# Optimization experiments

Measured on AMD Instinct MI355X. Metric: run time of the kernel, lower is better.

The kernel has to match this reference:

```python
import jax, jax.numpy as jnp
import numpy as np

K = 1024      # num_embeddings
D = 256       # embedding_dim
BETA = 0.25


def setup_inputs() -> dict:
    key = jax.random.key(0)
    k1, k2 = jax.random.split(key)
    z = jax.random.normal(k1, (4, D, 16, 32, 32), dtype=jnp.float32)
    # matches torch init: uniform(-1/K, 1/K)
    embedding = jax.random.uniform(k2, (K, D), dtype=jnp.float32,
                                   minval=-1.0 / K, maxval=1.0 / K)
    return {"z": z, "embedding": embedding}


def reference(z, embedding):
    # z: (B, C, Dd, H, W) with C == D
    z_perm = jnp.transpose(z, (0, 2, 3, 4, 1))          # (B, Dd, H, W, C)
    flat = z_perm.reshape(-1, D)                        # (N, D)

    dist = (jnp.sum(flat * flat, axis=1, keepdims=True)
            + jnp.sum(embedding * embedding, axis=1)
            - 2.0 * flat @ embedding.T)
    indices_flat = jnp.argmin(dist, axis=1)             # (N,)

    # one-hot @ embedding == direct gather
    z_q_flat = embedding[indices_flat]                  # (N, D)
    z_q = z_q_flat.reshape(z_perm.shape)

    commitment_loss = jnp.mean((z_perm - jax.lax.stop_gradient(z_q)) ** 2)
    vq_loss = BETA * commitment_loss

    # straight-through estimator
    z_q_st = z_perm + jax.lax.stop_gradient(z_q - z_perm)
    z_q_out = jnp.transpose(z_q_st, (0, 4, 1, 2, 3))    # back to (B, C, Dd, H, W)

    # perplexity from assignment histogram
    n = flat.shape[0]
    counts = jnp.zeros((K,), dtype=flat.dtype).at[indices_flat].add(1.0)
    avg_probs = counts / n
    perplexity = jnp.exp(-jnp.sum(avg_probs * jnp.log(avg_probs + 1e-10)))

    indices = indices_flat.reshape(z_perm.shape[:-1])   # (B, Dd, H, W)
    return z_q_out, vq_loss, indices, perplexity
```

## Files before the change

kernel.cpp:

```cpp
#include <hip/hip_runtime.h>

#define Dd 256
#define Kc 1024
#define SPATIAL 16384
#define NROWS 65536
#define NELEM 16777216
#define LOSS_OFF 16777216
#define IDX_OFF  16777217
#define PERP_OFF (16777217 + 65536)
#define MARGIN 3.5e-4f

typedef _Float16 f16x8 __attribute__((ext_vector_type(8)));
typedef _Float16 f16x2 __attribute__((ext_vector_type(2)));
typedef float f32x4 __attribute__((ext_vector_type(4)));


__global__ __launch_bounds__(256) void prep2_kernel(const float* __restrict__ emb,
                                                    _Float16* __restrict__ ef,
                                                    float* __restrict__ se) {
  const int j = blockIdx.x, c = threadIdx.x;
  float v = emb[j * Dd + c];
  ef[j * Dd + c] = (_Float16)(v * 1024.0f);
  double s = (double)v * (double)v;
  #pragma unroll
  for (int off = 32; off; off >>= 1) s += __shfl_down(s, off, 64);
  __shared__ double ws4[4];
  if ((threadIdx.x & 63) == 0) ws4[threadIdx.x >> 6] = s;
  __syncthreads();
  if (threadIdx.x == 0) se[j] = (float)(ws4[0] + ws4[1] + ws4[2] + ws4[3]);
}

__global__ __launch_bounds__(256, 2) void prefilter2_kernel(const float* __restrict__ z,
                                                            const _Float16* __restrict__ ef,
                                                            const float* __restrict__ se,
                                                            float* __restrict__ sx,
                                                            float* __restrict__ rowmin,
                                                            int* __restrict__ candcount,
                                                            int* __restrict__ cand_g) {
  __shared__ _Float16 As[32 * 272];
  __shared__ double sxp[8][32];
  __shared__ float selds[Kc];
  __shared__ int cnts[32];
  __shared__ int cands[32][8];
  __shared__ float rminw[4][32];
  __shared__ float rthr[32];

  const int tid = threadIdx.x;
  const int n0 = blockIdx.x * 32;
  const int b = n0 >> 14, s0 = n0 & 16383;
  const float* zb = z + (size_t)b * (Dd * SPATIAL) + s0;

  {
    const int r = tid & 31, cp = tid >> 5;
    double acc = 0.0;
    #pragma unroll 8
    for (int c = cp * 32; c < cp * 32 + 32; ++c) {
      const float v = zb[(size_t)c * SPATIAL + r];
      As[r * 272 + c] = (_Float16)v;
      acc += (double)v * (double)v;
    }
    sxp[cp][r] = acc;
  }
  #pragma unroll
  for (int i = 0; i < 4; ++i) selds[tid + 256 * i] = se[tid + 256 * i];
  if (tid < 32) cnts[tid] = 0;
  __syncthreads();
  if (tid < 32) {
    double s = 0.0;
    #pragma unroll
    for (int p = 0; p < 8; ++p) s += sxp[p][tid];
    sx[n0 + tid] = (float)s;
  }

  const int w = tid >> 6, lane = tid & 63, q = lane >> 4, l15 = lane & 15;
  const int colbase = w * 256;

  f16x8 Afrag[2][8];
  #pragma unroll
  for (int rt = 0; rt < 2; ++rt)
    #pragma unroll
    for (int kk = 0; kk < 8; ++kk)
      Afrag[rt][kk] = *(const f16x8*)(&As[(rt * 16 + l15) * 272 + kk * 32 + q * 8]);

  const _Float16* efb = ef + (size_t)(colbase + l15) * Dd + q * 8;

  float rmin8[8];
  #pragma unroll
  for (int i = 0; i < 8; ++i) rmin8[i] = 3.4e38f;
  f16x2 scst[16][4];

  #pragma unroll
  for (int ct = 0; ct < 16; ++ct) {
    const _Float16* bp = efb + (size_t)ct * 16 * Dd;
    f16x8 B[8];
    #pragma unroll
    for (int kk = 0; kk < 8; ++kk) B[kk] = *(const f16x8*)(bp + kk * 32);
    f32x4 a0 = {0.f, 0.f, 0.f, 0.f}, a1 = {0.f, 0.f, 0.f, 0.f};
    #pragma unroll
    for (int kk = 0; kk < 8; ++kk) {
      a0 = __builtin_amdgcn_mfma_f32_16x16x32_f16(Afrag[0][kk], B[kk], a0, 0, 0, 0);
      a1 = __builtin_amdgcn_mfma_f32_16x16x32_f16(Afrag[1][kk], B[kk], a1, 0, 0, 0);
    }
    const float sec = selds[colbase + ct * 16 + l15];
    #pragma unroll
    for (int reg = 0; reg < 4; ++reg) {
      const float sc0 = fmaf(-0.001953125f, a0[reg], sec);
      const float sc1 = fmaf(-0.001953125f, a1[reg], sec);
      rmin8[reg]     = fminf(rmin8[reg], sc0);
      rmin8[reg + 4] = fminf(rmin8[reg + 4], sc1);
      scst[ct][reg] = (f16x2){(_Float16)sc0, (_Float16)sc1};
    }
  }

  #pragma unroll
  for (int m = 1; m <= 8; m <<= 1)
    #pragma unroll
    for (int i = 0; i < 8; ++i) rmin8[i] = fminf(rmin8[i], __shfl_xor(rmin8[i], m, 64));
  if (l15 == 0) {
    #pragma unroll
    for (int reg = 0; reg < 4; ++reg) {
      rminw[w][q * 4 + reg] = rmin8[reg];
      rminw[w][16 + q * 4 + reg] = rmin8[4 + reg];
    }
  }
  __syncthreads();
  if (tid < 32) {
    const float m = fminf(fminf(rminw[0][tid], rminw[1][tid]),
                          fminf(rminw[2][tid], rminw[3][tid]));
    rowmin[n0 + tid] = m;
    rthr[tid] = m + MARGIN;
  }
  __syncthreads();

  float thr0[4], thr1[4];
  #pragma unroll
  for (int reg = 0; reg < 4; ++reg) {
    thr0[reg] = rthr[q * 4 + reg];
    thr1[reg] = rthr[16 + q * 4 + reg];
  }
  #pragma unroll
  for (int ct = 0; ct < 16; ++ct) {
    const int col = colbase + ct * 16 + l15;
    #pragma unroll
    for (int reg = 0; reg < 4; ++reg) {
      if ((float)scst[ct][reg][0] < thr0[reg]) {
        const int pos = atomicAdd(&cnts[q * 4 + reg], 1);
        if (pos < 8) cands[q * 4 + reg][pos] = col;
      }
      if ((float)scst[ct][reg][1] < thr1[reg]) {
        const int pos = atomicAdd(&cnts[16 + q * 4 + reg], 1);
        if (pos < 8) cands[16 + q * 4 + reg][pos] = col;
      }
    }
  }
  __syncthreads();
  if (tid < 32) candcount[n0 + tid] = cnts[tid];
  cand_g[(size_t)(n0 + (tid >> 3)) * 8 + (tid & 7)] = cands[tid >> 3][tid & 7];
}

__global__ __launch_bounds__(256) void resolve_easy_kernel(const int* __restrict__ candcount,
                                                           const int* __restrict__ cand_g,
                                                           const float* __restrict__ sx,
                                                           const float* __restrict__ rowmin,
                                                           float* __restrict__ out_idx_f,
                                                           int* __restrict__ idx_i,
                                                           int* __restrict__ counts,
                                                           int* __restrict__ hardcnt,
                                                           int* __restrict__ hardlist,
                                                           double* __restrict__ loss_sum) {
  const int tid = threadIdx.x;
  const int n = blockIdx.x * 256 + tid;
  const int cnt = candcount[n];
  double lp = 0.0;
  if (cnt == 1) {
    const int j = cand_g[(size_t)n * 8];
    idx_i[n] = j;
    out_idx_f[n] = (float)j;
    atomicAdd(&counts[j], 1);
    lp = (double)sx[n] + (double)rowmin[n];
  } else {
    const int pos = atomicAdd(hardcnt, 1);
    hardlist[pos] = n;
  }
  #pragma unroll
  for (int off = 32; off; off >>= 1) lp += __shfl_down(lp, off, 64);
  __shared__ double dred[4];
  if ((tid & 63) == 0) dred[tid >> 6] = lp;
  __syncthreads();
  if (tid == 0) atomicAdd(loss_sum, dred[0] + dred[1] + dred[2] + dred[3]);
}

__global__ __launch_bounds__(256) void resolve_hard_kernel(const float* __restrict__ z,
                                                           const float* __restrict__ emb,
                                                           const float* __restrict__ se,
                                                           const float* __restrict__ sx,
                                                           const int* __restrict__ candcount,
                                                           const int* __restrict__ cand_g,
                                                           const int* __restrict__ hardcnt,
                                                           const int* __restrict__ hardlist,
                                                           float* __restrict__ out_idx_f,
                                                           int* __restrict__ idx_i,
                                                           int* __restrict__ counts,
                                                           double* __restrict__ loss_sum) {
  __shared__ float xs[4][256];
  const int tid = threadIdx.x, w = tid >> 6, lane = tid & 63;
  const int hc = *hardcnt;
  const int nw = gridDim.x * 4;
  double wloss = 0.0;
  for (int i = blockIdx.x * 4 + w; i < hc; i += nw) {
    const int n = hardlist[i];
    const int b = n >> 14, s = n & 16383;
    #pragma unroll
    for (int ro = 0; ro < 4; ++ro)
      xs[w][ro * 64 + lane] =
          z[(size_t)b * (Dd * SPATIAL) + (size_t)(ro * 64 + lane) * SPATIAL + s];
    asm volatile("s_waitcnt lgkmcnt(0) vmcnt(0)" ::: "memory");
    const int cnt = candcount[n];
    const float sxn = sx[n];
    float scb = 3.4e38f;
    int jb = 0x7fffffff;
    if (cnt <= 8) {
      if (lane < cnt) {
        jb = cand_g[(size_t)n * 8 + lane];
        const float4* ep = (const float4*)(emb + (size_t)jb * Dd);
        float acc = 0.f;
        #pragma unroll 8
        for (int kk = 0; kk < 64; ++kk) {
          const float4 e4 = ep[kk];
          const float* xp = &xs[w][kk * 4];
          acc = fmaf(xp[0], e4.x, acc);
          acc = fmaf(xp[1], e4.y, acc);
          acc = fmaf(xp[2], e4.z, acc);
          acc = fmaf(xp[3], e4.w, acc);
        }
        const float t1 = sxn + se[jb];
        scb = t1 - 2.0f * acc;
      }
    } else {
      for (int jj = 0; jj < 16; ++jj) {
        const int j = lane * 16 + jj;
        const float4* ep = (const float4*)(emb + (size_t)j * Dd);
        float acc = 0.f;
        #pragma unroll 8
        for (int kk = 0; kk < 64; ++kk) {
          const float4 e4 = ep[kk];
          const float* xp = &xs[w][kk * 4];
          acc = fmaf(xp[0], e4.x, acc);
          acc = fmaf(xp[1], e4.y, acc);
          acc = fmaf(xp[2], e4.z, acc);
          acc = fmaf(xp[3], e4.w, acc);
        }
        const float t1 = sxn + se[j];
        const float sc = t1 - 2.0f * acc;
        if (sc < scb) { scb = sc; jb = j; }
      }
    }
    #pragma unroll
    for (int m = 1; m <= 32; m <<= 1) {
      const float so = __shfl_xor(scb, m, 64);
      const int jo = __shfl_xor(jb, m, 64);
      if (so < scb || (so == scb && jo < jb)) { scb = so; jb = jo; }
    }
    if (lane == 0) {
      idx_i[n] = jb;
      out_idx_f[n] = (float)jb;
      atomicAdd(&counts[jb], 1);
      wloss += (double)sxn + (double)scb;
    }
  }
  if (lane == 0) atomicAdd(loss_sum, wloss);
}

__global__ __launch_bounds__(256) void phase2c_kernel(const float* __restrict__ emb,
                                                      const int* __restrict__ idx_i,
                                                      float* __restrict__ out_zq) {
  __shared__ float els[64 * 257];
  __shared__ int sidx[64];
  const int tid = threadIdx.x;
  const int blk = blockIdx.x, b = blk >> 8, s0 = (blk & 255) << 6;
  if (tid < 64) sidx[tid] = idx_i[b * SPATIAL + s0 + tid];
  __syncthreads();
  {
    const int rr = tid >> 2, p = tid & 3;
    const float* ep = emb + (size_t)sidx[rr] * Dd + p * 64;
    float* dl = els + rr * 257 + p * 64;
    #pragma unroll
    for (int i = 0; i < 64; i += 4) {
      const float4 e4 = *(const float4*)(ep + i);
      dl[i] = e4.x; dl[i + 1] = e4.y; dl[i + 2] = e4.z; dl[i + 3] = e4.w;
    }
  }
  __syncthreads();
  const int s = tid & 63, coff = tid >> 6;
  const size_t zb = (size_t)b * (Dd * SPATIAL);
  #pragma unroll 4
  for (int c = coff; c < Dd; c += 4)
    out_zq[zb + (size_t)c * SPATIAL + s0 + s] = els[s * 257 + c];
}

__global__ __launch_bounds__(256) void finalize_kernel(const int* __restrict__ counts,
                                                       const double* __restrict__ loss_sum,
                                                       float* __restrict__ out) {
  const int tid = threadIdx.x;
  double local = 0.0;
  for (int k = tid; k < Kc; k += 256) {
    const double p = (double)counts[k] / (double)NROWS;
    local += p * log(p + 1e-10);
  }
  #pragma unroll
  for (int off = 32; off; off >>= 1) local += __shfl_down(local, off, 64);
  __shared__ double dred[4];
  if ((tid & 63) == 0) dred[tid >> 6] = local;
  __syncthreads();
  if (tid == 0) {
    const double H = dred[0] + dred[1] + dred[2] + dred[3];
    out[PERP_OFF] = (float)exp(-H);
    out[LOSS_OFF] = (float)(0.25 * loss_sum[0] / (double)NELEM);
  }
}


__global__ __launch_bounds__(256) void prep_kernel(const float* __restrict__ emb,
                                                   float* __restrict__ eT,
                                                   float* __restrict__ se) {
  const int j = blockIdx.x, c = threadIdx.x;
  float v = emb[j * Dd + c];
  eT[c * Kc + j] = v;
  double s = (double)v * (double)v;
  #pragma unroll
  for (int off = 32; off; off >>= 1) s += __shfl_down(s, off, 64);
  __shared__ double ws4[4];
  if ((threadIdx.x & 63) == 0) ws4[threadIdx.x >> 6] = s;
  __syncthreads();
  if (threadIdx.x == 0) se[j] = (float)(ws4[0] + ws4[1] + ws4[2] + ws4[3]);
}

__global__ __launch_bounds__(256) void sx_kernel(const float* __restrict__ z,
                                                 float* __restrict__ sx) {
  __shared__ double part[4][64];
  const int tid = threadIdx.x, r = tid & 63, cg = tid >> 6;
  const int blk = blockIdx.x, b = blk >> 8, s0 = (blk & 255) << 6;
  const float* zb = z + (size_t)b * (Dd * SPATIAL);
  double acc = 0.0;
  for (int c = cg * 64; c < cg * 64 + 64; ++c) {
    const float v = zb[(size_t)c * SPATIAL + s0 + r];
    acc += (double)v * (double)v;
  }
  part[cg][r] = acc;
  __syncthreads();
  if (tid < 64)
    sx[b * SPATIAL + s0 + tid] =
        (float)(part[0][tid] + part[1][tid] + part[2][tid] + part[3][tid]);
}

__global__ __launch_bounds__(256) void argmin_kernel(const float* __restrict__ z,
                                                     const float* __restrict__ eT,
                                                     const float* __restrict__ se,
                                                     const float* __restrict__ sx,
                                                     float* __restrict__ out_idx_f,
                                                     int* __restrict__ idx_i,
                                                     int* __restrict__ counts) {
  __shared__ float As[32 * 64];
  __shared__ float Bs[32 * 64];
  __shared__ float ses[Kc];
  __shared__ float sxs[64];
  __shared__ float redS1[64 * 16];
  __shared__ int   redI1[64 * 16];
  const int tid = threadIdx.x, tc = tid & 15, tr = tid >> 4;
  const int blk = blockIdx.x, b = blk >> 8, s0 = (blk & 255) << 6;
  const float* zb = z + (size_t)b * (Dd * SPATIAL);
  #pragma unroll
  for (int i = 0; i < 4; ++i) ses[tid + 256 * i] = se[tid + 256 * i];
  if (tid < 64) sxs[tid] = sx[b * SPATIAL + s0 + tid];
  float s1[4]; int j1[4];
  #pragma unroll
  for (int r = 0; r < 4; ++r) { s1[r] = 3.4e38f; j1[r] = 0; }
  for (int j0 = 0; j0 < Kc; j0 += 64) {
    float acc[4][4];
    #pragma unroll
    for (int rr = 0; rr < 4; ++rr)
      #pragma unroll
      for (int cc = 0; cc < 4; ++cc) acc[rr][cc] = 0.0f;
    for (int c0 = 0; c0 < Dd; c0 += 32) {
      __syncthreads();
      #pragma unroll
      for (int i = 0; i < 8; ++i) {
        const int e = i * 256 + tid, ci = e >> 6, r = e & 63;
        As[e] = zb[(size_t)(c0 + ci) * SPATIAL + s0 + r];
        Bs[e] = eT[(c0 + ci) * Kc + j0 + r];
      }
      __syncthreads();
      #pragma unroll
      for (int d = 0; d < 32; ++d) {
        const float4 av = *reinterpret_cast<const float4*>(&As[d * 64 + 4 * tr]);
        const float4 bv = *reinterpret_cast<const float4*>(&Bs[d * 64 + 4 * tc]);
        const float aa[4] = {av.x, av.y, av.z, av.w};
        const float bb[4] = {bv.x, bv.y, bv.z, bv.w};
        #pragma unroll
        for (int rr = 0; rr < 4; ++rr)
          #pragma unroll
          for (int cc = 0; cc < 4; ++cc)
            acc[rr][cc] = fmaf(aa[rr], bb[cc], acc[rr][cc]);
      }
    }
    #pragma unroll
    for (int rr = 0; rr < 4; ++rr) {
      const float sxr = sxs[4 * tr + rr];
      #pragma unroll
      for (int cc = 0; cc < 4; ++cc) {
        const int j = j0 + 4 * tc + cc;
        const float t1 = sxr + ses[j];
        const float s = t1 - 2.0f * acc[rr][cc];
        if (s < s1[rr] || (s == s1[rr] && j < j1[rr])) { s1[rr] = s; j1[rr] = j; }
      }
    }
  }
  #pragma unroll
  for (int rr = 0; rr < 4; ++rr) {
    redS1[(4 * tr + rr) * 16 + tc] = s1[rr];
    redI1[(4 * tr + rr) * 16 + tc] = j1[rr];
  }
  __syncthreads();
  if (tid < 64) {
    float bs = redS1[tid * 16];
    int bj = redI1[tid * 16];
    #pragma unroll
    for (int t = 1; t < 16; ++t) {
      const float a1 = redS1[tid * 16 + t];
      const int aj = redI1[tid * 16 + t];
      if (a1 < bs || (a1 == bs && aj < bj)) { bs = a1; bj = aj; }
    }
    const int n = b * SPATIAL + s0 + tid;
    out_idx_f[n] = (float)bj;
    idx_i[n] = bj;
    atomicAdd(&counts[bj], 1);
  }
}

__global__ __launch_bounds__(256) void phase2_kernel(const float* __restrict__ z,
                                                     const float* __restrict__ eT,
                                                     const int* __restrict__ idx_i,
                                                     float* __restrict__ out_zq,
                                                     double* __restrict__ loss_sum) {
  __shared__ int sidx[64];
  __shared__ double dred[4];
  const int tid = threadIdx.x;
  const int blk = blockIdx.x, b = blk >> 8, s0 = (blk & 255) << 6;
  if (tid < 64) sidx[tid] = idx_i[b * SPATIAL + s0 + tid];
  __syncthreads();
  const int s = tid & 63, coff = tid >> 6;
  const size_t zb = (size_t)b * (Dd * SPATIAL);
  const int myidx = sidx[s];
  double lsum = 0.0;
  for (int c = coff; c < Dd; c += 4) {
    const size_t off = zb + (size_t)c * SPATIAL + s0 + s;
    const float zv = z[off];
    const float zq = eT[c * Kc + myidx];
    out_zq[off] = zv + (zq - zv);
    const float d = zv - zq;
    lsum += (double)d * (double)d;
  }
  #pragma unroll
  for (int off = 32; off; off >>= 1) lsum += __shfl_down(lsum, off, 64);
  if ((tid & 63) == 0) dred[tid >> 6] = lsum;
  __syncthreads();
  if (tid == 0) atomicAdd(loss_sum, dred[0] + dred[1] + dred[2] + dred[3]);
}


extern "C" void kernel_launch(void* const* d_in, const int* in_sizes, int n_in,
                              void* d_out, int out_size, void* d_ws, size_t ws_size,
                              hipStream_t stream) {
  const float* z   = (const float*)d_in[0];
  const float* emb = (const float*)d_in[1];
  float* out = (float*)d_out;
  char* ws = (char*)d_ws;

  const size_t OFF_SE   = 8192;
  const size_t OFF_SX   = 12288;
  const size_t OFF_EF   = 274432;
  const size_t OFF_RM   = 798720;
  const size_t OFF_IDX  = 1060864;
  const size_t OFF_CCT  = 1323008;
  const size_t OFF_CAND = 1585152;
  const size_t OFF_HARD = 3682304;
  const size_t NEED     = 3944448;

  double* loss_sum = (double*)(ws + 0);
  int*    hardcnt  = (int*)(ws + 8);
  int*    counts   = (int*)(ws + 256);

  hipMemsetAsync(d_ws, 0, 8192, stream);

  if (ws_size >= NEED) {
    float*    se        = (float*)(ws + OFF_SE);
    float*    sx        = (float*)(ws + OFF_SX);
    _Float16* ef        = (_Float16*)(ws + OFF_EF);
    float*    rowmin    = (float*)(ws + OFF_RM);
    int*      idx_i     = (int*)(ws + OFF_IDX);
    int*      candcount = (int*)(ws + OFF_CCT);
    int*      cand_g    = (int*)(ws + OFF_CAND);
    int*      hardlist  = (int*)(ws + OFF_HARD);

    prep2_kernel<<<Kc, 256, 0, stream>>>(emb, ef, se);
    prefilter2_kernel<<<2048, 256, 0, stream>>>(z, ef, se, sx, rowmin,
                                                candcount, cand_g);
    resolve_easy_kernel<<<256, 256, 0, stream>>>(candcount, cand_g, sx, rowmin,
                                                 out + IDX_OFF, idx_i, counts,
                                                 hardcnt, hardlist, loss_sum);
    resolve_hard_kernel<<<256, 256, 0, stream>>>(z, emb, se, sx, candcount, cand_g,
                                                 hardcnt, hardlist, out + IDX_OFF,
                                                 idx_i, counts, loss_sum);
    phase2c_kernel<<<1024, 256, 0, stream>>>(emb, idx_i, out);
    finalize_kernel<<<1, 256, 0, stream>>>(counts, loss_sum, out);
  } else {
    float* eT    = (float*)(ws + 8192);
    float* se    = (float*)(ws + 8192 + 1048576);
    float* sx    = (float*)(ws + 8192 + 1048576 + 4096);
    int*   idx_i = (int*)(ws + 8192 + 1048576 + 4096 + 262144);

    prep_kernel<<<Kc, 256, 0, stream>>>(emb, eT, se);
    sx_kernel<<<1024, 256, 0, stream>>>(z, sx);
    argmin_kernel<<<1024, 256, 0, stream>>>(z, eT, se, sx, out + IDX_OFF, idx_i, counts);
    phase2_kernel<<<1024, 256, 0, stream>>>(z, eT, idx_i, out, loss_sum);
    finalize_kernel<<<1, 256, 0, stream>>>(counts, loss_sum, out);
  }
}
```

Measured before the change: 325.6 us.

## Recompute MFMA scores instead of storing, fuse easy-resolve into prefilter

```diff
diff --git a/kernel.cpp b/kernel.cpp
--- a/kernel.cpp
+++ b/kernel.cpp
@@ -9,9 +9,9 @@
 #define IDX_OFF  16777217
 #define PERP_OFF (16777217 + 65536)
 #define MARGIN 3.5e-4f
+#define ASTR 264
 
 typedef _Float16 f16x8 __attribute__((ext_vector_type(8)));
-typedef _Float16 f16x2 __attribute__((ext_vector_type(2)));
 typedef float f32x4 __attribute__((ext_vector_type(4)));
 
 
@@ -30,20 +30,26 @@
   if (threadIdx.x == 0) se[j] = (float)(ws4[0] + ws4[1] + ws4[2] + ws4[3]);
 }
 
-__global__ __launch_bounds__(256, 2) void prefilter2_kernel(const float* __restrict__ z,
+__global__ __launch_bounds__(256, 4) void prefilter4_kernel(const float* __restrict__ z,
                                                             const _Float16* __restrict__ ef,
                                                             const float* __restrict__ se,
                                                             float* __restrict__ sx,
-                                                            float* __restrict__ rowmin,
-                                                            int* __restrict__ candcount,
-                                                            int* __restrict__ cand_g) {
-  __shared__ _Float16 As[32 * 272];
+                                                            float* __restrict__ out_idx_f,
+                                                            int* __restrict__ idx_i,
+                                                            int* __restrict__ counts,
+                                                            int* __restrict__ hardcnt,
+                                                            int* __restrict__ hardlist,
+                                                            int* __restrict__ cand_g,
+                                                            double* __restrict__ loss_sum) {
+  __shared__ _Float16 As[32 * ASTR];
   __shared__ double sxp[8][32];
   __shared__ float selds[Kc];
+  __shared__ float sxl[32];
+  __shared__ float rminb[32];
+  __shared__ float rthr[32];
+  __shared__ float rminw[4][32];
   __shared__ int cnts[32];
   __shared__ int cands[32][8];
-  __shared__ float rminw[4][32];
-  __shared__ float rthr[32];
 
   const int tid = threadIdx.x;
   const int n0 = blockIdx.x * 32;
@@ -56,7 +62,7 @@
     #pragma unroll 8
     for (int c = cp * 32; c < cp * 32 + 32; ++c) {
       const float v = zb[(size_t)c * SPATIAL + r];
-      As[r * 272 + c] = (_Float16)v;
+      As[r * ASTR + c] = (_Float16)v;
       acc += (double)v * (double)v;
     }
     sxp[cp][r] = acc;
@@ -69,6 +75,7 @@
     double s = 0.0;
     #pragma unroll
     for (int p = 0; p < 8; ++p) s += sxp[p][tid];
+    sxl[tid] = (float)s;
     sx[n0 + tid] = (float)s;
   }
 
@@ -80,14 +87,13 @@
   for (int rt = 0; rt < 2; ++rt)
     #pragma unroll
     for (int kk = 0; kk < 8; ++kk)
-      Afrag[rt][kk] = *(const f16x8*)(&As[(rt * 16 + l15) * 272 + kk * 32 + q * 8]);
+      Afrag[rt][kk] = *(const f16x8*)(&As[(rt * 16 + l15) * ASTR + kk * 32 + q * 8]);
 
   const _Float16* efb = ef + (size_t)(colbase + l15) * Dd + q * 8;
 
   float rmin8[8];
   #pragma unroll
   for (int i = 0; i < 8; ++i) rmin8[i] = 3.4e38f;
-  f16x2 scst[16][4];
 
   #pragma unroll
   for (int ct = 0; ct < 16; ++ct) {
@@ -104,11 +110,8 @@
     const float sec = selds[colbase + ct * 16 + l15];
     #pragma unroll
     for (int reg = 0; reg < 4; ++reg) {
-      const float sc0 = fmaf(-0.001953125f, a0[reg], sec);
-      const float sc1 = fmaf(-0.001953125f, a1[reg], sec);
-      rmin8[reg]     = fminf(rmin8[reg], sc0);
-      rmin8[reg + 4] = fminf(rmin8[reg + 4], sc1);
-      scst[ct][reg] = (f16x2){(_Float16)sc0, (_Float16)sc1};
+      rmin8[reg]     = fminf(rmin8[reg],     fmaf(-0.001953125f, a0[reg], sec));
+      rmin8[reg + 4] = fminf(rmin8[reg + 4], fmaf(-0.001953125f, a1[reg], sec));
     }
   }
 
@@ -127,7 +130,7 @@
   if (tid < 32) {
     const float m = fminf(fminf(rminw[0][tid], rminw[1][tid]),
                           fminf(rminw[2][tid], rminw[3][tid]));
-    rowmin[n0 + tid] = m;
+    rminb[tid] = m;
     rthr[tid] = m + MARGIN;
   }
   __syncthreads();
@@ -140,64 +143,63 @@
   }
   #pragma unroll
   for (int ct = 0; ct < 16; ++ct) {
+    const _Float16* bp = efb + (size_t)ct * 16 * Dd;
+    f16x8 B[8];
+    #pragma unroll
+    for (int kk = 0; kk < 8; ++kk) B[kk] = *(const f16x8*)(bp + kk * 32);
+    f32x4 a0 = {0.f, 0.f, 0.f, 0.f}, a1 = {0.f, 0.f, 0.f, 0.f};
+    #pragma unroll
+    for (int kk = 0; kk < 8; ++kk) {
+      a0 = __builtin_amdgcn_mfma_f32_16x16x32_f16(Afrag[0][kk], B[kk], a0, 0, 0, 0);
+      a1 = __builtin_amdgcn_mfma_f32_16x16x32_f16(Afrag[1][kk], B[kk], a1, 0, 0, 0);
+    }
     const int col = colbase + ct * 16 + l15;
+    const float sec = selds[col];
     #pragma unroll
     for (int reg = 0; reg < 4; ++reg) {
-      if ((float)scst[ct][reg][0] < thr0[reg]) {
+      if (fmaf(-0.001953125f, a0[reg], sec) < thr0[reg]) {
         const int pos = atomicAdd(&cnts[q * 4 + reg], 1);
         if (pos < 8) cands[q * 4 + reg][pos] = col;
       }
-      if ((float)scst[ct][reg][1] < thr1[reg]) {
+      if (fmaf(-0.001953125f, a1[reg], sec) < thr1[reg]) {
         const int pos = atomicAdd(&cnts[16 + q * 4 + reg], 1);
         if (pos < 8) cands[16 + q * 4 + reg][pos] = col;
       }
     }
   }
   __syncthreads();
-  if (tid < 32) candcount[n0 + tid] = cnts[tid];
-  cand_g[(size_t)(n0 + (tid >> 3)) * 8 + (tid & 7)] = cands[tid >> 3][tid & 7];
-}
-
-__global__ __launch_bounds__(256) void resolve_easy_kernel(const int* __restrict__ candcount,
-                                                           const int* __restrict__ cand_g,
-                                                           const float* __restrict__ sx,
-                                                           const float* __restrict__ rowmin,
-                                                           float* __restrict__ out_idx_f,
-                                                           int* __restrict__ idx_i,
-                                                           int* __restrict__ counts,
-                                                           int* __restrict__ hardcnt,
-                                                           int* __restrict__ hardlist,
-                                                           double* __restrict__ loss_sum) {
-  const int tid = threadIdx.x;
-  const int n = blockIdx.x * 256 + tid;
-  const int cnt = candcount[n];
+
   double lp = 0.0;
-  if (cnt == 1) {
-    const int j = cand_g[(size_t)n * 8];
-    idx_i[n] = j;
-    out_idx_f[n] = (float)j;
-    atomicAdd(&counts[j], 1);
-    lp = (double)sx[n] + (double)rowmin[n];
-  } else {
-    const int pos = atomicAdd(hardcnt, 1);
-    hardlist[pos] = n;
-  }
-  #pragma unroll
-  for (int off = 32; off; off >>= 1) lp += __shfl_down(lp, off, 64);
-  __shared__ double dred[4];
-  if ((tid & 63) == 0) dred[tid >> 6] = lp;
-  __syncthreads();
-  if (tid == 0) atomicAdd(loss_sum, dred[0] + dred[1] + dred[2] + dred[3]);
+  if (tid < 32) {
+    const int n = n0 + tid;
+    const int cnt = cnts[tid];
+    if (cnt == 1) {
+      const int j = cands[tid][0];
+      idx_i[n] = j;
+      out_idx_f[n] = (float)j;
+      atomicAdd(&counts[j], 1);
+      lp = (double)sxl[tid] + (double)rminb[tid];
+    } else {
+      const int pos = atomicAdd(hardcnt, 1);
+      hardlist[pos] = (min(cnt, 9) << 20) | n;
+      const int m = min(cnt, 8);
+      for (int i = 0; i < m; ++i) cand_g[(size_t)n * 8 + i] = cands[tid][i];
+    }
+  }
+  if (tid < 64) {
+    #pragma unroll
+    for (int off = 32; off; off >>= 1) lp += __shfl_down(lp, off, 64);
+    if (tid == 0) atomicAdd(loss_sum, lp);
+  }
 }
 
 __global__ __launch_bounds__(256) void resolve_hard_kernel(const float* __restrict__ z,
                                                            const float* __restrict__ emb,
                                                            const float* __restrict__ se,
                                                            const float* __restrict__ sx,
-                                                           const int* __restrict__ candcount,
-                                                           const int* __restrict__ cand_g,
                                                            const int* __restrict__ hardcnt,
                                                            const int* __restrict__ hardlist,
+                                                           const int* __restrict__ cand_g,
                                                            float* __restrict__ out_idx_f,
                                                            int* __restrict__ idx_i,
                                                            int* __restrict__ counts,
@@ -208,14 +210,15 @@
   const int nw = gridDim.x * 4;
   double wloss = 0.0;
   for (int i = blockIdx.x * 4 + w; i < hc; i += nw) {
-    const int n = hardlist[i];
+    const int e = hardlist[i];
+    const int n = e & 0xFFFFF;
+    const int cnt = e >> 20;
     const int b = n >> 14, s = n & 16383;
     #pragma unroll
     for (int ro = 0; ro < 4; ++ro)
       xs[w][ro * 64 + lane] =
           z[(size_t)b * (Dd * SPATIAL) + (size_t)(ro * 64 + lane) * SPATIAL + s];
     asm volatile("s_waitcnt lgkmcnt(0) vmcnt(0)" ::: "memory");
-    const int cnt = candcount[n];
     const float sxn = sx[n];
     float scb = 3.4e38f;
     int jb = 0x7fffffff;
@@ -479,12 +482,10 @@
   const size_t OFF_SE   = 8192;
   const size_t OFF_SX   = 12288;
   const size_t OFF_EF   = 274432;
-  const size_t OFF_RM   = 798720;
-  const size_t OFF_IDX  = 1060864;
-  const size_t OFF_CCT  = 1323008;
-  const size_t OFF_CAND = 1585152;
-  const size_t OFF_HARD = 3682304;
-  const size_t NEED     = 3944448;
+  const size_t OFF_IDX  = 798720;
+  const size_t OFF_CAND = 1060864;
+  const size_t OFF_HARD = 3158016;
+  const size_t NEED     = 3420160;
 
   double* loss_sum = (double*)(ws + 0);
   int*    hardcnt  = (int*)(ws + 8);
@@ -493,24 +494,20 @@
   hipMemsetAsync(d_ws, 0, 8192, stream);
 
   if (ws_size >= NEED) {
-    float*    se        = (float*)(ws + OFF_SE);
-    float*    sx        = (float*)(ws + OFF_SX);
-    _Float16* ef        = (_Float16*)(ws + OFF_EF);
-    float*    rowmin    = (float*)(ws + OFF_RM);
-    int*      idx_i     = (int*)(ws + OFF_IDX);
-    int*      candcount = (int*)(ws + OFF_CCT);
-    int*      cand_g    = (int*)(ws + OFF_CAND);
-    int*      hardlist  = (int*)(ws + OFF_HARD);
+    float*    se       = (float*)(ws + OFF_SE);
+    float*    sx       = (float*)(ws + OFF_SX);
+    _Float16* ef       = (_Float16*)(ws + OFF_EF);
+    int*      idx_i    = (int*)(ws + OFF_IDX);
+    int*      cand_g   = (int*)(ws + OFF_CAND);
+    int*      hardlist = (int*)(ws + OFF_HARD);
 
     prep2_kernel<<<Kc, 256, 0, stream>>>(emb, ef, se);
-    prefilter2_kernel<<<2048, 256, 0, stream>>>(z, ef, se, sx, rowmin,
-                                                candcount, cand_g);
-    resolve_easy_kernel<<<256, 256, 0, stream>>>(candcount, cand_g, sx, rowmin,
-                                                 out + IDX_OFF, idx_i, counts,
-                                                 hardcnt, hardlist, loss_sum);
-    resolve_hard_kernel<<<256, 256, 0, stream>>>(z, emb, se, sx, candcount, cand_g,
-                                                 hardcnt, hardlist, out + IDX_OFF,
-                                                 idx_i, counts, loss_sum);
+    prefilter4_kernel<<<2048, 256, 0, stream>>>(z, ef, se, sx, out + IDX_OFF,
+                                                idx_i, counts, hardcnt, hardlist,
+                                                cand_g, loss_sum);
+    resolve_hard_kernel<<<256, 256, 0, stream>>>(z, emb, se, sx, hardcnt, hardlist,
+                                                 cand_g, out + IDX_OFF, idx_i,
+                                                 counts, loss_sum);
     phase2c_kernel<<<1024, 256, 0, stream>>>(emb, idx_i, out);
     finalize_kernel<<<1, 256, 0, stream>>>(counts, loss_sum, out);
   } else {
```

Measured after the change: 398.8 us. +22.5%, slower.
